# Optimization experiments

Measured on AMD Instinct MI355X. Metric: run time of the kernel, lower is better.

Reference implementation:

```python
import jax, jax.numpy as jnp
import numpy as np

D = 1024   # dim_embedding
H = 16     # n_head
HD = D // H


def setup_inputs() -> dict:
    key = jax.random.key(0)
    ks = jax.random.split(key, 5)
    B, T = 2, 2048
    x = jax.random.normal(ks[0], (B, T, D), dtype=jnp.float32)
    e = jax.random.normal(ks[1], (B, T, D), dtype=jnp.float32)
    s = 0.02
    W_en = jax.random.normal(ks[2], (D, 2 * D), dtype=jnp.float32) * s   # c_attn_en (k,v from encoder)
    W_q = jax.random.normal(ks[3], (D, D), dtype=jnp.float32) * s        # c_attn (q from decoder)
    W_o = jax.random.normal(ks[4], (D, D), dtype=jnp.float32) * s        # c_proj
    return {"x": x, "e": e, "W_en": W_en, "W_q": W_q, "W_o": W_o}


def reference(x, e, W_en, W_q, W_o):
    B, T, C = e.shape
    kv = e @ W_en                       # [B,T,2C]
    k, v = jnp.split(kv, 2, axis=-1)    # [B,T,C] each
    q = x @ W_q                         # [B,T,C]
    # reshape to heads: [B,H,T,hd]
    q = q.reshape(B, T, H, HD).transpose(0, 2, 1, 3)
    k = k.reshape(B, T, H, HD).transpose(0, 2, 1, 3)
    v = v.reshape(B, T, H, HD).transpose(0, 2, 1, 3)
    att = jnp.einsum("bhqd,bhkd->bhqk", q, k) * (1.0 / jnp.sqrt(jnp.float32(HD)))
    att = jax.nn.softmax(att, axis=-1)  # dropout=0 (eval)
    y = jnp.einsum("bhqk,bhkd->bhqd", att, v)
    y = y.transpose(0, 2, 1, 3).reshape(B, T, C)
    return y @ W_o
```

## Files before the change

### kernel.cpp

```cpp
#include <hip/hip_runtime.h>

typedef unsigned short u16;
typedef unsigned int u32;
typedef __bf16 bf16x8 __attribute__((ext_vector_type(8)));
typedef float f32x4 __attribute__((ext_vector_type(4)));
typedef float f32x16 __attribute__((ext_vector_type(16)));

#define D_EMB 1024
#define T_SEQ 2048
#define NH 16
#define HD 64

#define GLB(p) ((const __attribute__((address_space(1))) unsigned int*)(p))
#define LDSP(p) ((__attribute__((address_space(3))) unsigned int*)(p))

__device__ __forceinline__ u16 f2bf(float f) {
  union { float f; unsigned u; } c; c.f = f;
  unsigned u = c.u;
  unsigned r = (u + 0x7FFFu + ((u >> 16) & 1u)) >> 16;
  return (u16)r;
}
__device__ __forceinline__ u32 fbits(float f) {
  union { float f; unsigned u; } c; c.f = f; return c.u;
}

__global__ __launch_bounds__(256) void prep_kernel(
    const float* __restrict__ x, const float* __restrict__ e,
    const float* __restrict__ W_q, const float* __restrict__ W_en, const float* __restrict__ W_o,
    u16* __restrict__ xb, u16* __restrict__ eb,
    u16* __restrict__ Wqt, u16* __restrict__ Went, u16* __restrict__ Wot) {
  __shared__ float tile[32][33];
  const int bid = blockIdx.x, tid = threadIdx.x;
  if (bid < 8192) {
    const float* in = (bid < 4096) ? x : e;
    u16* out = (bid < 4096) ? xb : eb;
    int i = (bid & 4095) * 256 + tid;
    float4 v = reinterpret_cast<const float4*>(in)[i];
    ushort4 o;
    o.x = f2bf(v.x); o.y = f2bf(v.y); o.z = f2bf(v.z); o.w = f2bf(v.w);
    reinterpret_cast<ushort4*>(out)[i] = o;
    return;
  }
  const float* in; u16* out; int K, N, bx, by;
  int rem = bid - 8192;
  if (rem < 1024)      { in = W_q;  out = Wqt;  K = 1024; N = 1024; bx = rem & 31; by = rem >> 5; }
  else if (rem < 3072) { int r2 = rem - 1024; in = W_en; out = Went; K = 1024; N = 2048; bx = r2 & 63; by = r2 >> 6; }
  else                 { int r3 = rem - 3072; in = W_o;  out = Wot;  K = 1024; N = 1024; bx = r3 & 31; by = r3 >> 5; }
  int tx = tid & 31, ty = tid >> 5;
  int n0 = bx * 32, k0 = by * 32;
#pragma unroll
  for (int s = 0; s < 4; s++)
    tile[ty + 8 * s][tx] = in[(size_t)(k0 + ty + 8 * s) * N + n0 + tx];
  __syncthreads();
#pragma unroll
  for (int s = 0; s < 4; s++)
    out[(size_t)(n0 + ty + 8 * s) * K + k0 + tx] = f2bf(tile[tx][ty + 8 * s]);
}

__global__ __launch_bounds__(256) void proj_kernel(
    const u16* __restrict__ xb, const u16* __restrict__ eb,
    const u16* __restrict__ Wqt, const u16* __restrict__ Went,
    u16* __restrict__ qw, u16* __restrict__ kw, u16* __restrict__ vTw) {
  __shared__ u16 Al0[128 * 32], Bl0[128 * 32];
  __shared__ u16 Al1[128 * 32], Bl1[128 * 32];
  const int tid = threadIdx.x;
  const int nb = blockIdx.x, mb = blockIdx.y;
  const int wave = tid >> 6, lane = tid & 63;
  const int ln15 = lane & 15, quad = lane >> 4;
  const int wm = wave & 1, wn = wave >> 1;

  const u16* A = (nb < 8) ? xb : eb;
  const u16* Wt = (nb < 8) ? (Wqt + (size_t)nb * 128 * D_EMB)
                           : (Went + ((size_t)nb * 128 - D_EMB) * D_EMB);

  const int srow = lane >> 2, sch = lane & 3;
  const int gch = sch ^ ((srow >> 1) & 3);
  const u16* gA = A + (size_t)(mb * 128 + wave * 32 + srow) * D_EMB + gch * 8;
  const u16* gB = Wt + (size_t)(wave * 32 + srow) * D_EMB + gch * 8;

  auto stage = [&](int kb, u16* AL, u16* BL) {
    char* lA = (char*)AL + wave * 2048;
    char* lB = (char*)BL + wave * 2048;
#pragma unroll
    for (int it = 0; it < 2; it++) {
      __builtin_amdgcn_global_load_lds(GLB(gA + (size_t)it * 16 * D_EMB + kb), LDSP(lA + it * 1024), 16, 0, 0);
      __builtin_amdgcn_global_load_lds(GLB(gB + (size_t)it * 16 * D_EMB + kb), LDSP(lB + it * 1024), 16, 0, 0);
    }
  };

  f32x4 acc[4][4] = {};

  auto compute = [&](const u16* AL, const u16* BL) {
    bf16x8 af[4], bfr[4];
#pragma unroll
    for (int mt = 0; mt < 4; mt++) {
      int r = wm * 64 + mt * 16 + ln15;
      af[mt] = *reinterpret_cast<const bf16x8*>(&AL[r * 32 + ((quad ^ ((r >> 1) & 3)) * 8)]);
    }
#pragma unroll
    for (int nt = 0; nt < 4; nt++) {
      int r = wn * 64 + nt * 16 + ln15;
      bfr[nt] = *reinterpret_cast<const bf16x8*>(&BL[r * 32 + ((quad ^ ((r >> 1) & 3)) * 8)]);
    }
#pragma unroll
    for (int mt = 0; mt < 4; mt++)
#pragma unroll
      for (int nt = 0; nt < 4; nt++)
        acc[mt][nt] = __builtin_amdgcn_mfma_f32_16x16x32_bf16(af[mt], bfr[nt], acc[mt][nt], 0, 0, 0);
  };

  stage(0, Al0, Bl0);
  for (int kb = 0; kb < D_EMB; kb += 64) {
    __syncthreads();
    stage(kb + 32, Al1, Bl1);
    compute(Al0, Bl0);
    __syncthreads();
    if (kb + 64 < D_EMB) stage(kb + 64, Al0, Bl0);
    compute(Al1, Bl1);
  }

  const float QSCL = 0.125f * 1.44269504f;
#pragma unroll
  for (int mt = 0; mt < 4; mt++) {
#pragma unroll
    for (int nt = 0; nt < 4; nt++) {
#pragma unroll
      for (int i = 0; i < 4; i++) {
        int rr = mb * 128 + wm * 64 + mt * 16 + quad * 4 + i;
        int c  = nb * 128 + wn * 64 + nt * 16 + ln15;
        float v = acc[mt][nt][i];
        int b = rr >> 11, t = rr & 2047;
        if (c < D_EMB) {
          int h = c >> 6, d = c & 63;
          qw[(((size_t)(b * NH + h)) * T_SEQ + t) * HD + d] = f2bf(v * QSCL);
        } else if (c < 2 * D_EMB) {
          int cc = c - D_EMB; int h = cc >> 6, d = cc & 63;
          kw[(((size_t)(b * NH + h)) * T_SEQ + t) * HD + d] = f2bf(v);
        } else {
          int cc = c - 2 * D_EMB; int h = cc >> 6, d = cc & 63;
          vTw[(((size_t)(b * NH + h)) * HD + d) * T_SEQ + t] = f2bf(v);
        }
      }
    }
  }
}

__global__ __launch_bounds__(256) void attn_kernel(
    const u16* __restrict__ q, const u16* __restrict__ k,
    const u16* __restrict__ vT, u16* __restrict__ y) {
  __shared__ u16 Kl0[64][64], Vl0[64][64];
  __shared__ u16 Kl1[64][64], Vl1[64][64];
  __shared__ u16 Pl[4][32][64];

  const int bh = blockIdx.y;
  const int qt = blockIdx.x;
  const int tid = threadIdx.x;
  const int wave = tid >> 6, lane = tid & 63;
  const int q32 = lane & 31, hi = lane >> 5;
  const int b = bh >> 4, h = bh & 15;

  const int qrow = qt * 128 + wave * 32 + q32;
  const u16* qbase = q + ((size_t)bh * T_SEQ + qrow) * HD;
  bf16x8 qf[4];
#pragma unroll
  for (int s = 0; s < 4; s++)
    qf[s] = *reinterpret_cast<const bf16x8*>(qbase + s * 16 + hi * 8);

  f32x16 o2[2] = {};
  float lp = 0.f;

  const int srow = (lane >> 3) & 7;
  const int gch  = (lane & 7) ^ srow;
  const u16* kg0 = k  + ((size_t)bh * T_SEQ + wave * 16 + srow) * HD + gch * 8;
  const u16* vg0 = vT + ((size_t)bh * HD + wave * 16 + srow) * T_SEQ + gch * 8;

  auto issue_dma = [&](int t, u16 (*KL)[64], u16 (*VL)[64]) {
    char* klb = (char*)KL + wave * 2048;
    char* vlb = (char*)VL + wave * 2048;
    const u16* kp = kg0 + (size_t)t * 64 * HD;
    const u16* vp = vg0 + t * 64;
    __builtin_amdgcn_global_load_lds(GLB(kp),             LDSP(klb),        16, 0, 0);
    __builtin_amdgcn_global_load_lds(GLB(kp + 8 * HD),    LDSP(klb + 1024), 16, 0, 0);
    __builtin_amdgcn_global_load_lds(GLB(vp),             LDSP(vlb),        16, 0, 0);
    __builtin_amdgcn_global_load_lds(GLB(vp + 8 * T_SEQ), LDSP(vlb + 1024), 16, 0, 0);
  };

  auto body = [&](const u16 (*KL)[64], const u16 (*VL)[64]) {
    f32x16 s2[2] = {};
#pragma unroll
    for (int s = 0; s < 4; s++)
#pragma unroll
      for (int kt2 = 0; kt2 < 2; kt2++) {
        int r = kt2 * 32 + q32;
        bf16x8 kf = *reinterpret_cast<const bf16x8*>(&KL[r][(((s * 2 + hi) ^ (r & 7)) * 8)]);
        s2[kt2] = __builtin_amdgcn_mfma_f32_32x32x16_bf16(kf, qf[s], s2[kt2], 0, 0, 0);
      }

#pragma unroll
    for (int kt2 = 0; kt2 < 2; kt2++)
#pragma unroll
      for (int g = 0; g < 4; g++) {
        float p0 = __builtin_amdgcn_exp2f(s2[kt2][4 * g + 0]);
        float p1 = __builtin_amdgcn_exp2f(s2[kt2][4 * g + 1]);
        float p2 = __builtin_amdgcn_exp2f(s2[kt2][4 * g + 2]);
        float p3 = __builtin_amdgcn_exp2f(s2[kt2][4 * g + 3]);
        lp += (p0 + p1) + (p2 + p3);
        u32 dw0 = __builtin_amdgcn_perm(fbits(p1), fbits(p0), 0x07060302u);
        u32 dw1 = __builtin_amdgcn_perm(fbits(p3), fbits(p2), 0x07060302u);
        int phys = (kt2 * 4 + g) ^ (q32 & 7);
        *reinterpret_cast<uint2*>(&Pl[wave][q32][phys * 8 + 4 * hi]) = make_uint2(dw0, dw1);
      }
    asm volatile("s_waitcnt lgkmcnt(0)" ::: "memory");

#pragma unroll
    for (int s = 0; s < 4; s++) {
      bf16x8 pf = *reinterpret_cast<const bf16x8*>(
          &Pl[wave][q32][(((s * 2 + hi) ^ (q32 & 7)) * 8)]);
#pragma unroll
      for (int dt = 0; dt < 2; dt++) {
        int r = dt * 32 + q32;
        bf16x8 vf = *reinterpret_cast<const bf16x8*>(&VL[r][(((s * 2 + hi) ^ (r & 7)) * 8)]);
        o2[dt] = __builtin_amdgcn_mfma_f32_32x32x16_bf16(vf, pf, o2[dt], 0, 0, 0);
      }
    }
  };

  issue_dma(0, Kl0, Vl0);
  for (int t = 0; t < 32; t += 2) {
    __syncthreads();
    issue_dma(t + 1, Kl1, Vl1);
    body(Kl0, Vl0);
    __syncthreads();
    if (t + 2 < 32) issue_dma(t + 2, Kl0, Vl0);
    body(Kl1, Vl1);
  }

  lp += __shfl_xor(lp, 32, 64);
  const float inv = 1.0f / lp;

  const size_t ybase = ((size_t)b * T_SEQ + qrow) * D_EMB + h * 64;
#pragma unroll
  for (int dt = 0; dt < 2; dt++)
#pragma unroll
    for (int g = 0; g < 4; g++) {
      u16 b0 = f2bf(o2[dt][4 * g + 0] * inv), b1 = f2bf(o2[dt][4 * g + 1] * inv);
      u16 b2 = f2bf(o2[dt][4 * g + 2] * inv), b3 = f2bf(o2[dt][4 * g + 3] * inv);
      u32 dw0 = (u32)b0 | ((u32)b1 << 16);
      u32 dw1 = (u32)b2 | ((u32)b3 << 16);
      *reinterpret_cast<uint2*>(&y[ybase + dt * 32 + 8 * g + 4 * hi]) = make_uint2(dw0, dw1);
    }
}

__global__ __launch_bounds__(256) void oproj_kernel(
    const u16* __restrict__ yw, const u16* __restrict__ Wot, float* __restrict__ out) {
  __shared__ u16 Al0[64 * 32], Al1[64 * 32];
  __shared__ u16 Bl0[128 * 32], Bl1[128 * 32];
  const int tid = threadIdx.x;
  const int nb = blockIdx.x, mb = blockIdx.y;
  const int wave = tid >> 6, lane = tid & 63;
  const int ln15 = lane & 15, quad = lane >> 4;
  const int wm = wave & 1, wn = wave >> 1;

  const int srow = lane >> 2, sch = lane & 3;
  const int gch = sch ^ ((srow >> 1) & 3);
  const u16* gA = yw  + (size_t)(mb * 64 + wave * 16 + srow) * D_EMB + gch * 8;
  const u16* gB = Wot + (size_t)(nb * 128 + wave * 32 + srow) * D_EMB + gch * 8;

  auto stage = [&](int kb, u16* AL, u16* BL) {
    char* lA = (char*)AL + wave * 1024;
    char* lB = (char*)BL + wave * 2048;
    __builtin_amdgcn_global_load_lds(GLB(gA + kb), LDSP(lA), 16, 0, 0);
#pragma unroll
    for (int it = 0; it < 2; it++)
      __builtin_amdgcn_global_load_lds(GLB(gB + (size_t)it * 16 * D_EMB + kb), LDSP(lB + it * 1024), 16, 0, 0);
  };

  f32x4 acc[2][4] = {};

  auto compute = [&](const u16* AL, const u16* BL) {
    bf16x8 af[2], bfr[4];
#pragma unroll
    for (int mt = 0; mt < 2; mt++) {
      int r = wm * 32 + mt * 16 + ln15;
      af[mt] = *reinterpret_cast<const bf16x8*>(&AL[r * 32 + ((quad ^ ((r >> 1) & 3)) * 8)]);
    }
#pragma unroll
    for (int nt = 0; nt < 4; nt++) {
      int r = wn * 64 + nt * 16 + ln15;
      bfr[nt] = *reinterpret_cast<const bf16x8*>(&BL[r * 32 + ((quad ^ ((r >> 1) & 3)) * 8)]);
    }
#pragma unroll
    for (int mt = 0; mt < 2; mt++)
#pragma unroll
      for (int nt = 0; nt < 4; nt++)
        acc[mt][nt] = __builtin_amdgcn_mfma_f32_16x16x32_bf16(af[mt], bfr[nt], acc[mt][nt], 0, 0, 0);
  };

  stage(0, Al0, Bl0);
  for (int kb = 0; kb < D_EMB; kb += 64) {
    __syncthreads();
    stage(kb + 32, Al1, Bl1);
    compute(Al0, Bl0);
    __syncthreads();
    if (kb + 64 < D_EMB) stage(kb + 64, Al0, Bl0);
    compute(Al1, Bl1);
  }

#pragma unroll
  for (int mt = 0; mt < 2; mt++)
#pragma unroll
    for (int nt = 0; nt < 4; nt++)
#pragma unroll
      for (int i = 0; i < 4; i++) {
        int rr = mb * 64 + wm * 32 + mt * 16 + quad * 4 + i;
        int c  = nb * 128 + wn * 64 + nt * 16 + ln15;
        out[(size_t)rr * D_EMB + c] = acc[mt][nt][i];
      }
}

extern "C" void kernel_launch(void* const* d_in, const int* in_sizes, int n_in,
                              void* d_out, int out_size, void* d_ws, size_t ws_size,
                              hipStream_t stream) {
  const float* x    = (const float*)d_in[0];
  const float* e    = (const float*)d_in[1];
  const float* W_en = (const float*)d_in[2];
  const float* W_q  = (const float*)d_in[3];
  const float* W_o  = (const float*)d_in[4];
  float* out = (float*)d_out;

  char* w = (char*)d_ws;
  u16* xb   = (u16*)(w);
  u16* eb   = (u16*)(w + (8u  << 20));
  u16* Wqt  = (u16*)(w + (16u << 20));
  u16* Went = (u16*)(w + (18u << 20));
  u16* Wot  = (u16*)(w + (22u << 20));
  u16* qw   = (u16*)(w + (24u << 20));
  u16* kw   = (u16*)(w + (32u << 20));
  u16* vT   = (u16*)(w + (40u << 20));
  u16* yw   = (u16*)(w + (48u << 20));

  prep_kernel<<<12288, 256, 0, stream>>>(x, e, W_q, W_en, W_o, xb, eb, Wqt, Went, Wot);
  proj_kernel<<<dim3(24, 32), 256, 0, stream>>>(xb, eb, Wqt, Went, qw, kw, vT);
  attn_kernel<<<dim3(T_SEQ / 128, 32), 256, 0, stream>>>(qw, kw, vT, yw);
  oproj_kernel<<<dim3(8, 64), 256, 0, stream>>>(yw, Wot, out);
}
```

Before: 203.3 us.

## Fuse prep, projection, attention and output projection into one persistent kernel

Replaces the four separate launches with a single persistent kernel of 768 blocks that runs each phase in turn, separated by software grid barriers built on atomic counters. The goal is to remove launch gaps and tail effects between the stages. This relies on all 768 blocks being co-resident (launch bounds of 3 blocks per CU with 48KB of shared memory each), and if that fails the kernel deadlocks. In the attention and output-projection phases only 512 of the 768 blocks do work, and the y buffer now reuses the xb workspace region.

```diff
diff --git a/kernel.cpp b/kernel.cpp
--- a/kernel.cpp
+++ b/kernel.cpp
@@ -10,6 +10,7 @@
 #define T_SEQ 2048
 #define NH 16
 #define HD 64
+#define GRID_N 768u
 
 #define GLB(p) ((const __attribute__((address_space(1))) unsigned int*)(p))
 #define LDSP(p) ((__attribute__((address_space(3))) unsigned int*)(p))
@@ -24,298 +25,309 @@
   union { float f; unsigned u; } c; c.f = f; return c.u;
 }
 
-__global__ __launch_bounds__(256) void prep_kernel(
+__device__ __forceinline__ void gridbar(u32* cnt, u32 target) {
+  __syncthreads();
+  if (threadIdx.x == 0) {
+    __hip_atomic_fetch_add(cnt, 1u, __ATOMIC_RELEASE, __HIP_MEMORY_SCOPE_AGENT);
+    while (__hip_atomic_load(cnt, __ATOMIC_ACQUIRE, __HIP_MEMORY_SCOPE_AGENT) < target)
+      __builtin_amdgcn_s_sleep(8);
+  }
+  __syncthreads();
+}
+
+__global__ __launch_bounds__(256, 3) void mega_kernel(
     const float* __restrict__ x, const float* __restrict__ e,
     const float* __restrict__ W_q, const float* __restrict__ W_en, const float* __restrict__ W_o,
     u16* __restrict__ xb, u16* __restrict__ eb,
-    u16* __restrict__ Wqt, u16* __restrict__ Went, u16* __restrict__ Wot) {
-  __shared__ float tile[32][33];
-  const int bid = blockIdx.x, tid = threadIdx.x;
-  if (bid < 8192) {
-    const float* in = (bid < 4096) ? x : e;
-    u16* out = (bid < 4096) ? xb : eb;
-    int i = (bid & 4095) * 256 + tid;
-    float4 v = reinterpret_cast<const float4*>(in)[i];
-    ushort4 o;
-    o.x = f2bf(v.x); o.y = f2bf(v.y); o.z = f2bf(v.z); o.w = f2bf(v.w);
-    reinterpret_cast<ushort4*>(out)[i] = o;
-    return;
-  }
-  const float* in; u16* out; int K, N, bx, by;
-  int rem = bid - 8192;
-  if (rem < 1024)      { in = W_q;  out = Wqt;  K = 1024; N = 1024; bx = rem & 31; by = rem >> 5; }
-  else if (rem < 3072) { int r2 = rem - 1024; in = W_en; out = Went; K = 1024; N = 2048; bx = r2 & 63; by = r2 >> 6; }
-  else                 { int r3 = rem - 3072; in = W_o;  out = Wot;  K = 1024; N = 1024; bx = r3 & 31; by = r3 >> 5; }
-  int tx = tid & 31, ty = tid >> 5;
-  int n0 = bx * 32, k0 = by * 32;
-#pragma unroll
-  for (int s = 0; s < 4; s++)
-    tile[ty + 8 * s][tx] = in[(size_t)(k0 + ty + 8 * s) * N + n0 + tx];
-  __syncthreads();
-#pragma unroll
-  for (int s = 0; s < 4; s++)
-    out[(size_t)(n0 + ty + 8 * s) * K + k0 + tx] = f2bf(tile[tx][ty + 8 * s]);
-}
-
-__global__ __launch_bounds__(256) void proj_kernel(
-    const u16* __restrict__ xb, const u16* __restrict__ eb,
-    const u16* __restrict__ Wqt, const u16* __restrict__ Went,
-    u16* __restrict__ qw, u16* __restrict__ kw, u16* __restrict__ vTw) {
-  __shared__ u16 Al0[128 * 32], Bl0[128 * 32];
-  __shared__ u16 Al1[128 * 32], Bl1[128 * 32];
+    u16* __restrict__ Wqt, u16* __restrict__ Went, u16* __restrict__ Wot,
+    u16* __restrict__ qw, u16* __restrict__ kw, u16* __restrict__ vTw,
+    u16* __restrict__ yw, float* __restrict__ out, u32* __restrict__ bar) {
+  __shared__ __align__(16) char smem[49152];
+  const int bid = blockIdx.x;
   const int tid = threadIdx.x;
-  const int nb = blockIdx.x, mb = blockIdx.y;
   const int wave = tid >> 6, lane = tid & 63;
   const int ln15 = lane & 15, quad = lane >> 4;
-  const int wm = wave & 1, wn = wave >> 1;
-
-  const u16* A = (nb < 8) ? xb : eb;
-  const u16* Wt = (nb < 8) ? (Wqt + (size_t)nb * 128 * D_EMB)
-                           : (Went + ((size_t)nb * 128 - D_EMB) * D_EMB);
-
-  const int srow = lane >> 2, sch = lane & 3;
-  const int gch = sch ^ ((srow >> 1) & 3);
-  const u16* gA = A + (size_t)(mb * 128 + wave * 32 + srow) * D_EMB + gch * 8;
-  const u16* gB = Wt + (size_t)(wave * 32 + srow) * D_EMB + gch * 8;
-
-  auto stage = [&](int kb, u16* AL, u16* BL) {
-    char* lA = (char*)AL + wave * 2048;
-    char* lB = (char*)BL + wave * 2048;
-#pragma unroll
-    for (int it = 0; it < 2; it++) {
-      __builtin_amdgcn_global_load_lds(GLB(gA + (size_t)it * 16 * D_EMB + kb), LDSP(lA + it * 1024), 16, 0, 0);
-      __builtin_amdgcn_global_load_lds(GLB(gB + (size_t)it * 16 * D_EMB + kb), LDSP(lB + it * 1024), 16, 0, 0);
-    }
-  };
-
-  f32x4 acc[4][4] = {};
-
-  auto compute = [&](const u16* AL, const u16* BL) {
-    bf16x8 af[4], bfr[4];
+
+  {
+    float* tile = (float*)smem;
+    for (u32 u = (u32)bid; u < 12288u; u += GRID_N) {
+      if (u < 8192u) {
+        const float* in = (u < 4096u) ? x : e;
+        u16* outp = (u < 4096u) ? xb : eb;
+        int i = (int)(u & 4095u) * 256 + tid;
+        float4 v = reinterpret_cast<const float4*>(in)[i];
+        ushort4 o;
+        o.x = f2bf(v.x); o.y = f2bf(v.y); o.z = f2bf(v.z); o.w = f2bf(v.w);
+        reinterpret_cast<ushort4*>(outp)[i] = o;
+      } else {
+        const float* in; u16* outp; int K, N, bx, by;
+        int rem = (int)u - 8192;
+        if (rem < 1024)      { in = W_q;  outp = Wqt;  K = 1024; N = 1024; bx = rem & 31; by = rem >> 5; }
+        else if (rem < 3072) { int r2 = rem - 1024; in = W_en; outp = Went; K = 1024; N = 2048; bx = r2 & 63; by = r2 >> 6; }
+        else                 { int r3 = rem - 3072; in = W_o;  outp = Wot;  K = 1024; N = 1024; bx = r3 & 31; by = r3 >> 5; }
+        int tx = tid & 31, ty = tid >> 5;
+        int n0 = bx * 32, k0 = by * 32;
+        __syncthreads();
+#pragma unroll
+        for (int s = 0; s < 4; s++)
+          tile[(ty + 8 * s) * 33 + tx] = in[(size_t)(k0 + ty + 8 * s) * N + n0 + tx];
+        __syncthreads();
+#pragma unroll
+        for (int s = 0; s < 4; s++)
+          outp[(size_t)(n0 + ty + 8 * s) * K + k0 + tx] = f2bf(tile[tx * 33 + ty + 8 * s]);
+      }
+    }
+  }
+  gridbar(bar, GRID_N);
+
+  {
+    u16* Al0 = (u16*)(smem);
+    u16* Bl0 = (u16*)(smem + 8192);
+    u16* Al1 = (u16*)(smem + 16384);
+    u16* Bl1 = (u16*)(smem + 24576);
+    const int nb = bid % 24, mb = bid / 24;
+    const int wm = wave & 1, wn = wave >> 1;
+
+    const u16* A = (nb < 8) ? xb : eb;
+    const u16* Wt = (nb < 8) ? (Wqt + (size_t)nb * 128 * D_EMB)
+                             : (Went + ((size_t)nb * 128 - D_EMB) * D_EMB);
+
+    const int srow = lane >> 2, sch = lane & 3;
+    const int gch = sch ^ ((srow >> 1) & 3);
+    const u16* gA = A + (size_t)(mb * 128 + wave * 32 + srow) * D_EMB + gch * 8;
+    const u16* gB = Wt + (size_t)(wave * 32 + srow) * D_EMB + gch * 8;
+
+    auto stage = [&](int kb, u16* AL, u16* BL) {
+      char* lA = (char*)AL + wave * 2048;
+      char* lB = (char*)BL + wave * 2048;
+#pragma unroll
+      for (int it = 0; it < 2; it++) {
+        __builtin_amdgcn_global_load_lds(GLB(gA + (size_t)it * 16 * D_EMB + kb), LDSP(lA + it * 1024), 16, 0, 0);
+        __builtin_amdgcn_global_load_lds(GLB(gB + (size_t)it * 16 * D_EMB + kb), LDSP(lB + it * 1024), 16, 0, 0);
+      }
+    };
+
+    f32x4 acc[4][4] = {};
+    auto compute = [&](const u16* AL, const u16* BL) {
+      bf16x8 af[4], bfr[4];
+#pragma unroll
+      for (int mt = 0; mt < 4; mt++) {
+        int r = wm * 64 + mt * 16 + ln15;
+        af[mt] = *reinterpret_cast<const bf16x8*>(&AL[r * 32 + ((quad ^ ((r >> 1) & 3)) * 8)]);
+      }
+#pragma unroll
+      for (int nt = 0; nt < 4; nt++) {
+        int r = wn * 64 + nt * 16 + ln15;
+        bfr[nt] = *reinterpret_cast<const bf16x8*>(&BL[r * 32 + ((quad ^ ((r >> 1) & 3)) * 8)]);
+      }
+#pragma unroll
+      for (int mt = 0; mt < 4; mt++)
+#pragma unroll
+        for (int nt = 0; nt < 4; nt++)
+          acc[mt][nt] = __builtin_amdgcn_mfma_f32_16x16x32_bf16(af[mt], bfr[nt], acc[mt][nt], 0, 0, 0);
+    };
+
+    stage(0, Al0, Bl0);
+    for (int kb = 0; kb < D_EMB; kb += 64) {
+      __syncthreads();
+      stage(kb + 32, Al1, Bl1);
+      compute(Al0, Bl0);
+      __syncthreads();
+      if (kb + 64 < D_EMB) stage(kb + 64, Al0, Bl0);
+      compute(Al1, Bl1);
+    }
+
+    const float QSCL = 0.125f * 1.44269504f;
 #pragma unroll
     for (int mt = 0; mt < 4; mt++) {
-      int r = wm * 64 + mt * 16 + ln15;
-      af[mt] = *reinterpret_cast<const bf16x8*>(&AL[r * 32 + ((quad ^ ((r >> 1) & 3)) * 8)]);
-    }
-#pragma unroll
-    for (int nt = 0; nt < 4; nt++) {
-      int r = wn * 64 + nt * 16 + ln15;
-      bfr[nt] = *reinterpret_cast<const bf16x8*>(&BL[r * 32 + ((quad ^ ((r >> 1) & 3)) * 8)]);
-    }
-#pragma unroll
-    for (int mt = 0; mt < 4; mt++)
+#pragma unroll
+      for (int nt = 0; nt < 4; nt++) {
+#pragma unroll
+        for (int i = 0; i < 4; i++) {
+          int rr = mb * 128 + wm * 64 + mt * 16 + quad * 4 + i;
+          int c  = nb * 128 + wn * 64 + nt * 16 + ln15;
+          float v = acc[mt][nt][i];
+          int b = rr >> 11, t = rr & 2047;
+          if (c < D_EMB) {
+            int h = c >> 6, d = c & 63;
+            qw[(((size_t)(b * NH + h)) * T_SEQ + t) * HD + d] = f2bf(v * QSCL);
+          } else if (c < 2 * D_EMB) {
+            int cc = c - D_EMB; int h = cc >> 6, d = cc & 63;
+            kw[(((size_t)(b * NH + h)) * T_SEQ + t) * HD + d] = f2bf(v);
+          } else {
+            int cc = c - 2 * D_EMB; int h = cc >> 6, d = cc & 63;
+            vTw[(((size_t)(b * NH + h)) * HD + d) * T_SEQ + t] = f2bf(v);
+          }
+        }
+      }
+    }
+  }
+  gridbar(bar, 2 * GRID_N);
+
+  if (bid < 512) {
+    u16 (*Kl0)[64] = (u16(*)[64])(smem);
+    u16 (*Vl0)[64] = (u16(*)[64])(smem + 8192);
+    u16 (*Kl1)[64] = (u16(*)[64])(smem + 16384);
+    u16 (*Vl1)[64] = (u16(*)[64])(smem + 24576);
+    u16* Pl = (u16*)(smem + 32768);
+
+    const int qt = bid & 15, bh = bid >> 4;
+    const int q32 = lane & 31, hi = lane >> 5;
+    const int b = bh >> 4, h = bh & 15;
+
+    const int qrow = qt * 128 + wave * 32 + q32;
+    const u16* qbase = qw + ((size_t)bh * T_SEQ + qrow) * HD;
+    bf16x8 qf[4];
+#pragma unroll
+    for (int s = 0; s < 4; s++)
+      qf[s] = *reinterpret_cast<const bf16x8*>(qbase + s * 16 + hi * 8);
+
+    f32x16 o2[2] = {};
+    float lp = 0.f;
+
+    const int srow = (lane >> 3) & 7;
+    const int gch  = (lane & 7) ^ srow;
+    const u16* kg0 = kw  + ((size_t)bh * T_SEQ + wave * 16 + srow) * HD + gch * 8;
+    const u16* vg0 = vTw + ((size_t)bh * HD + wave * 16 + srow) * T_SEQ + gch * 8;
+
+    auto issue_dma = [&](int t, u16 (*KL)[64], u16 (*VL)[64]) {
+      char* klb = (char*)KL + wave * 2048;
+      char* vlb = (char*)VL + wave * 2048;
+      const u16* kp = kg0 + (size_t)t * 64 * HD;
+      const u16* vp = vg0 + t * 64;
+      __builtin_amdgcn_global_load_lds(GLB(kp),             LDSP(klb),        16, 0, 0);
+      __builtin_amdgcn_global_load_lds(GLB(kp + 8 * HD),    LDSP(klb + 1024), 16, 0, 0);
+      __builtin_amdgcn_global_load_lds(GLB(vp),             LDSP(vlb),        16, 0, 0);
+      __builtin_amdgcn_global_load_lds(GLB(vp + 8 * T_SEQ), LDSP(vlb + 1024), 16, 0, 0);
+    };
+
+    auto body = [&](const u16 (*KL)[64], const u16 (*VL)[64]) {
+      f32x16 s2[2] = {};
+#pragma unroll
+      for (int s = 0; s < 4; s++)
+#pragma unroll
+        for (int kt2 = 0; kt2 < 2; kt2++) {
+          int r = kt2 * 32 + q32;
+          bf16x8 kf = *reinterpret_cast<const bf16x8*>(&KL[r][(((s * 2 + hi) ^ (r & 7)) * 8)]);
+          s2[kt2] = __builtin_amdgcn_mfma_f32_32x32x16_bf16(kf, qf[s], s2[kt2], 0, 0, 0);
+        }
+#pragma unroll
+      for (int kt2 = 0; kt2 < 2; kt2++)
+#pragma unroll
+        for (int g = 0; g < 4; g++) {
+          float p0 = __builtin_amdgcn_exp2f(s2[kt2][4 * g + 0]);
+          float p1 = __builtin_amdgcn_exp2f(s2[kt2][4 * g + 1]);
+          float p2 = __builtin_amdgcn_exp2f(s2[kt2][4 * g + 2]);
+          float p3 = __builtin_amdgcn_exp2f(s2[kt2][4 * g + 3]);
+          lp += (p0 + p1) + (p2 + p3);
+          u32 dw0 = __builtin_amdgcn_perm(fbits(p1), fbits(p0), 0x07060302u);
+          u32 dw1 = __builtin_amdgcn_perm(fbits(p3), fbits(p2), 0x07060302u);
+          int phys = (kt2 * 4 + g) ^ (q32 & 7);
+          *reinterpret_cast<uint2*>(&Pl[(wave * 32 + q32) * 64 + phys * 8 + 4 * hi]) = make_uint2(dw0, dw1);
+        }
+      asm volatile("s_waitcnt lgkmcnt(0)" ::: "memory");
+#pragma unroll
+      for (int s = 0; s < 4; s++) {
+        bf16x8 pf = *reinterpret_cast<const bf16x8*>(
+            &Pl[(wave * 32 + q32) * 64 + (((s * 2 + hi) ^ (q32 & 7)) * 8)]);
+#pragma unroll
+        for (int dt = 0; dt < 2; dt++) {
+          int r = dt * 32 + q32;
+          bf16x8 vf = *reinterpret_cast<const bf16x8*>(&VL[r][(((s * 2 + hi) ^ (r & 7)) * 8)]);
+          o2[dt] = __builtin_amdgcn_mfma_f32_32x32x16_bf16(vf, pf, o2[dt], 0, 0, 0);
+        }
+      }
+    };
+
+    issue_dma(0, Kl0, Vl0);
+    for (int t = 0; t < 32; t += 2) {
+      __syncthreads();
+      issue_dma(t + 1, Kl1, Vl1);
+      body(Kl0, Vl0);
+      __syncthreads();
+      if (t + 2 < 32) issue_dma(t + 2, Kl0, Vl0);
+      body(Kl1, Vl1);
+    }
+
+    lp += __shfl_xor(lp, 32, 64);
+    const float inv = 1.0f / lp;
+    const size_t ybase = ((size_t)b * T_SEQ + qrow) * D_EMB + h * 64;
+#pragma unroll
+    for (int dt = 0; dt < 2; dt++)
+#pragma unroll
+      for (int g = 0; g < 4; g++) {
+        u16 b0 = f2bf(o2[dt][4 * g + 0] * inv), b1 = f2bf(o2[dt][4 * g + 1] * inv);
+        u16 b2 = f2bf(o2[dt][4 * g + 2] * inv), b3 = f2bf(o2[dt][4 * g + 3] * inv);
+        u32 dw0 = (u32)b0 | ((u32)b1 << 16);
+        u32 dw1 = (u32)b2 | ((u32)b3 << 16);
+        *reinterpret_cast<uint2*>(&yw[ybase + dt * 32 + 8 * g + 4 * hi]) = make_uint2(dw0, dw1);
+      }
+  }
+  gridbar(bar, 3 * GRID_N);
+
+  if (bid < 512) {
+    u16* Al0 = (u16*)(smem);
+    u16* Al1 = (u16*)(smem + 4096);
+    u16* Bl0 = (u16*)(smem + 8192);
+    u16* Bl1 = (u16*)(smem + 16384);
+    const int nb = bid & 7, mb = bid >> 3;
+    const int wm = wave & 1, wn = wave >> 1;
+
+    const int srow = lane >> 2, sch = lane & 3;
+    const int gch = sch ^ ((srow >> 1) & 3);
+    const u16* gA = yw  + (size_t)(mb * 64 + wave * 16 + srow) * D_EMB + gch * 8;
+    const u16* gB = Wot + (size_t)(nb * 128 + wave * 32 + srow) * D_EMB + gch * 8;
+
+    auto stage = [&](int kb, u16* AL, u16* BL) {
+      char* lA = (char*)AL + wave * 1024;
+      char* lB = (char*)BL + wave * 2048;
+      __builtin_amdgcn_global_load_lds(GLB(gA + kb), LDSP(lA), 16, 0, 0);
+#pragma unroll
+      for (int it = 0; it < 2; it++)
+        __builtin_amdgcn_global_load_lds(GLB(gB + (size_t)it * 16 * D_EMB + kb), LDSP(lB + it * 1024), 16, 0, 0);
+    };
+
+    f32x4 acc[2][4] = {};
+    auto compute = [&](const u16* AL, const u16* BL) {
+      bf16x8 af[2], bfr[4];
+#pragma unroll
+      for (int mt = 0; mt < 2; mt++) {
+        int r = wm * 32 + mt * 16 + ln15;
+        af[mt] = *reinterpret_cast<const bf16x8*>(&AL[r * 32 + ((quad ^ ((r >> 1) & 3)) * 8)]);
+      }
+#pragma unroll
+      for (int nt = 0; nt < 4; nt++) {
+        int r = wn * 64 + nt * 16 + ln15;
+        bfr[nt] = *reinterpret_cast<const bf16x8*>(&BL[r * 32 + ((quad ^ ((r >> 1) & 3)) * 8)]);
+      }
+#pragma unroll
+      for (int mt = 0; mt < 2; mt++)
+#pragma unroll
+        for (int nt = 0; nt < 4; nt++)
+          acc[mt][nt] = __builtin_amdgcn_mfma_f32_16x16x32_bf16(af[mt], bfr[nt], acc[mt][nt], 0, 0, 0);
+    };
+
+    stage(0, Al0, Bl0);
+    for (int kb = 0; kb < D_EMB; kb += 64) {
+      __syncthreads();
+      stage(kb + 32, Al1, Bl1);
+      compute(Al0, Bl0);
+      __syncthreads();
+      if (kb + 64 < D_EMB) stage(kb + 64, Al0, Bl0);
+      compute(Al1, Bl1);
+    }
+
+#pragma unroll
+    for (int mt = 0; mt < 2; mt++)
 #pragma unroll
       for (int nt = 0; nt < 4; nt++)
-        acc[mt][nt] = __builtin_amdgcn_mfma_f32_16x16x32_bf16(af[mt], bfr[nt], acc[mt][nt], 0, 0, 0);
-  };
-
-  stage(0, Al0, Bl0);
-  for (int kb = 0; kb < D_EMB; kb += 64) {
-    __syncthreads();
-    stage(kb + 32, Al1, Bl1);
-    compute(Al0, Bl0);
-    __syncthreads();
-    if (kb + 64 < D_EMB) stage(kb + 64, Al0, Bl0);
-    compute(Al1, Bl1);
-  }
-
-  const float QSCL = 0.125f * 1.44269504f;
-#pragma unroll
-  for (int mt = 0; mt < 4; mt++) {
-#pragma unroll
-    for (int nt = 0; nt < 4; nt++) {
-#pragma unroll
-      for (int i = 0; i < 4; i++) {
-        int rr = mb * 128 + wm * 64 + mt * 16 + quad * 4 + i;
-        int c  = nb * 128 + wn * 64 + nt * 16 + ln15;
-        float v = acc[mt][nt][i];
-        int b = rr >> 11, t = rr & 2047;
-        if (c < D_EMB) {
-          int h = c >> 6, d = c & 63;
-          qw[(((size_t)(b * NH + h)) * T_SEQ + t) * HD + d] = f2bf(v * QSCL);
-        } else if (c < 2 * D_EMB) {
-          int cc = c - D_EMB; int h = cc >> 6, d = cc & 63;
-          kw[(((size_t)(b * NH + h)) * T_SEQ + t) * HD + d] = f2bf(v);
-        } else {
-          int cc = c - 2 * D_EMB; int h = cc >> 6, d = cc & 63;
-          vTw[(((size_t)(b * NH + h)) * HD + d) * T_SEQ + t] = f2bf(v);
-        }
-      }
-    }
-  }
-}
-
-__global__ __launch_bounds__(256) void attn_kernel(
-    const u16* __restrict__ q, const u16* __restrict__ k,
-    const u16* __restrict__ vT, u16* __restrict__ y) {
-  __shared__ u16 Kl0[64][64], Vl0[64][64];
-  __shared__ u16 Kl1[64][64], Vl1[64][64];
-  __shared__ u16 Pl[4][32][64];
-
-  const int bh = blockIdx.y;
-  const int qt = blockIdx.x;
-  const int tid = threadIdx.x;
-  const int wave = tid >> 6, lane = tid & 63;
-  const int q32 = lane & 31, hi = lane >> 5;
-  const int b = bh >> 4, h = bh & 15;
-
-  const int qrow = qt * 128 + wave * 32 + q32;
-  const u16* qbase = q + ((size_t)bh * T_SEQ + qrow) * HD;
-  bf16x8 qf[4];
-#pragma unroll
-  for (int s = 0; s < 4; s++)
-    qf[s] = *reinterpret_cast<const bf16x8*>(qbase + s * 16 + hi * 8);
-
-  f32x16 o2[2] = {};
-  float lp = 0.f;
-
-  const int srow = (lane >> 3) & 7;
-  const int gch  = (lane & 7) ^ srow;
-  const u16* kg0 = k  + ((size_t)bh * T_SEQ + wave * 16 + srow) * HD + gch * 8;
-  const u16* vg0 = vT + ((size_t)bh * HD + wave * 16 + srow) * T_SEQ + gch * 8;
-
-  auto issue_dma = [&](int t, u16 (*KL)[64], u16 (*VL)[64]) {
-    char* klb = (char*)KL + wave * 2048;
-    char* vlb = (char*)VL + wave * 2048;
-    const u16* kp = kg0 + (size_t)t * 64 * HD;
-    const u16* vp = vg0 + t * 64;
-    __builtin_amdgcn_global_load_lds(GLB(kp),             LDSP(klb),        16, 0, 0);
-    __builtin_amdgcn_global_load_lds(GLB(kp + 8 * HD),    LDSP(klb + 1024), 16, 0, 0);
-    __builtin_amdgcn_global_load_lds(GLB(vp),             LDSP(vlb),        16, 0, 0);
-    __builtin_amdgcn_global_load_lds(GLB(vp + 8 * T_SEQ), LDSP(vlb + 1024), 16, 0, 0);
-  };
-
-  auto body = [&](const u16 (*KL)[64], const u16 (*VL)[64]) {
-    f32x16 s2[2] = {};
-#pragma unroll
-    for (int s = 0; s < 4; s++)
-#pragma unroll
-      for (int kt2 = 0; kt2 < 2; kt2++) {
-        int r = kt2 * 32 + q32;
-        bf16x8 kf = *reinterpret_cast<const bf16x8*>(&KL[r][(((s * 2 + hi) ^ (r & 7)) * 8)]);
-        s2[kt2] = __builtin_amdgcn_mfma_f32_32x32x16_bf16(kf, qf[s], s2[kt2], 0, 0, 0);
-      }
-
-#pragma unroll
-    for (int kt2 = 0; kt2 < 2; kt2++)
-#pragma unroll
-      for (int g = 0; g < 4; g++) {
-        float p0 = __builtin_amdgcn_exp2f(s2[kt2][4 * g + 0]);
-        float p1 = __builtin_amdgcn_exp2f(s2[kt2][4 * g + 1]);
-        float p2 = __builtin_amdgcn_exp2f(s2[kt2][4 * g + 2]);
-        float p3 = __builtin_amdgcn_exp2f(s2[kt2][4 * g + 3]);
-        lp += (p0 + p1) + (p2 + p3);
-        u32 dw0 = __builtin_amdgcn_perm(fbits(p1), fbits(p0), 0x07060302u);
-        u32 dw1 = __builtin_amdgcn_perm(fbits(p3), fbits(p2), 0x07060302u);
-        int phys = (kt2 * 4 + g) ^ (q32 & 7);
-        *reinterpret_cast<uint2*>(&Pl[wave][q32][phys * 8 + 4 * hi]) = make_uint2(dw0, dw1);
-      }
-    asm volatile("s_waitcnt lgkmcnt(0)" ::: "memory");
-
-#pragma unroll
-    for (int s = 0; s < 4; s++) {
-      bf16x8 pf = *reinterpret_cast<const bf16x8*>(
-          &Pl[wave][q32][(((s * 2 + hi) ^ (q32 & 7)) * 8)]);
-#pragma unroll
-      for (int dt = 0; dt < 2; dt++) {
-        int r = dt * 32 + q32;
-        bf16x8 vf = *reinterpret_cast<const bf16x8*>(&VL[r][(((s * 2 + hi) ^ (r & 7)) * 8)]);
-        o2[dt] = __builtin_amdgcn_mfma_f32_32x32x16_bf16(vf, pf, o2[dt], 0, 0, 0);
-      }
-    }
-  };
-
-  issue_dma(0, Kl0, Vl0);
-  for (int t = 0; t < 32; t += 2) {
-    __syncthreads();
-    issue_dma(t + 1, Kl1, Vl1);
-    body(Kl0, Vl0);
-    __syncthreads();
-    if (t + 2 < 32) issue_dma(t + 2, Kl0, Vl0);
-    body(Kl1, Vl1);
-  }
-
-  lp += __shfl_xor(lp, 32, 64);
-  const float inv = 1.0f / lp;
-
-  const size_t ybase = ((size_t)b * T_SEQ + qrow) * D_EMB + h * 64;
-#pragma unroll
-  for (int dt = 0; dt < 2; dt++)
-#pragma unroll
-    for (int g = 0; g < 4; g++) {
-      u16 b0 = f2bf(o2[dt][4 * g + 0] * inv), b1 = f2bf(o2[dt][4 * g + 1] * inv);
-      u16 b2 = f2bf(o2[dt][4 * g + 2] * inv), b3 = f2bf(o2[dt][4 * g + 3] * inv);
-      u32 dw0 = (u32)b0 | ((u32)b1 << 16);
-      u32 dw1 = (u32)b2 | ((u32)b3 << 16);
-      *reinterpret_cast<uint2*>(&y[ybase + dt * 32 + 8 * g + 4 * hi]) = make_uint2(dw0, dw1);
-    }
-}
-
-__global__ __launch_bounds__(256) void oproj_kernel(
-    const u16* __restrict__ yw, const u16* __restrict__ Wot, float* __restrict__ out) {
-  __shared__ u16 Al0[64 * 32], Al1[64 * 32];
-  __shared__ u16 Bl0[128 * 32], Bl1[128 * 32];
-  const int tid = threadIdx.x;
-  const int nb = blockIdx.x, mb = blockIdx.y;
-  const int wave = tid >> 6, lane = tid & 63;
-  const int ln15 = lane & 15, quad = lane >> 4;
-  const int wm = wave & 1, wn = wave >> 1;
-
-  const int srow = lane >> 2, sch = lane & 3;
-  const int gch = sch ^ ((srow >> 1) & 3);
-  const u16* gA = yw  + (size_t)(mb * 64 + wave * 16 + srow) * D_EMB + gch * 8;
-  const u16* gB = Wot + (size_t)(nb * 128 + wave * 32 + srow) * D_EMB + gch * 8;
-
-  auto stage = [&](int kb, u16* AL, u16* BL) {
-    char* lA = (char*)AL + wave * 1024;
-    char* lB = (char*)BL + wave * 2048;
-    __builtin_amdgcn_global_load_lds(GLB(gA + kb), LDSP(lA), 16, 0, 0);
-#pragma unroll
-    for (int it = 0; it < 2; it++)
-      __builtin_amdgcn_global_load_lds(GLB(gB + (size_t)it * 16 * D_EMB + kb), LDSP(lB + it * 1024), 16, 0, 0);
-  };
-
-  f32x4 acc[2][4] = {};
-
-  auto compute = [&](const u16* AL, const u16* BL) {
-    bf16x8 af[2], bfr[4];
-#pragma unroll
-    for (int mt = 0; mt < 2; mt++) {
-      int r = wm * 32 + mt * 16 + ln15;
-      af[mt] = *reinterpret_cast<const bf16x8*>(&AL[r * 32 + ((quad ^ ((r >> 1) & 3)) * 8)]);
-    }
-#pragma unroll
-    for (int nt = 0; nt < 4; nt++) {
-      int r = wn * 64 + nt * 16 + ln15;
-      bfr[nt] = *reinterpret_cast<const bf16x8*>(&BL[r * 32 + ((quad ^ ((r >> 1) & 3)) * 8)]);
-    }
-#pragma unroll
-    for (int mt = 0; mt < 2; mt++)
-#pragma unroll
-      for (int nt = 0; nt < 4; nt++)
-        acc[mt][nt] = __builtin_amdgcn_mfma_f32_16x16x32_bf16(af[mt], bfr[nt], acc[mt][nt], 0, 0, 0);
-  };
-
-  stage(0, Al0, Bl0);
-  for (int kb = 0; kb < D_EMB; kb += 64) {
-    __syncthreads();
-    stage(kb + 32, Al1, Bl1);
-    compute(Al0, Bl0);
-    __syncthreads();
-    if (kb + 64 < D_EMB) stage(kb + 64, Al0, Bl0);
-    compute(Al1, Bl1);
-  }
-
-#pragma unroll
-  for (int mt = 0; mt < 2; mt++)
-#pragma unroll
-    for (int nt = 0; nt < 4; nt++)
-#pragma unroll
-      for (int i = 0; i < 4; i++) {
-        int rr = mb * 64 + wm * 32 + mt * 16 + quad * 4 + i;
-        int c  = nb * 128 + wn * 64 + nt * 16 + ln15;
-        out[(size_t)rr * D_EMB + c] = acc[mt][nt][i];
-      }
+#pragma unroll
+        for (int i = 0; i < 4; i++) {
+          int rr = mb * 64 + wm * 32 + mt * 16 + quad * 4 + i;
+          int c  = nb * 128 + wn * 64 + nt * 16 + ln15;
+          out[(size_t)rr * D_EMB + c] = acc[mt][nt][i];
+        }
+  }
 }
 
 extern "C" void kernel_launch(void* const* d_in, const int* in_sizes, int n_in,
@@ -330,6 +342,7 @@
 
   char* w = (char*)d_ws;
   u16* xb   = (u16*)(w);
+  u16* yw   = (u16*)(w);
   u16* eb   = (u16*)(w + (8u  << 20));
   u16* Wqt  = (u16*)(w + (16u << 20));
   u16* Went = (u16*)(w + (18u << 20));
@@ -337,10 +350,10 @@
   u16* qw   = (u16*)(w + (24u << 20));
   u16* kw   = (u16*)(w + (32u << 20));
   u16* vT   = (u16*)(w + (40u << 20));
-  u16* yw   = (u16*)(w + (48u << 20));
-
-  prep_kernel<<<12288, 256, 0, stream>>>(x, e, W_q, W_en, W_o, xb, eb, Wqt, Went, Wot);
-  proj_kernel<<<dim3(24, 32), 256, 0, stream>>>(xb, eb, Wqt, Went, qw, kw, vT);
-  attn_kernel<<<dim3(T_SEQ / 128, 32), 256, 0, stream>>>(qw, kw, vT, yw);
-  oproj_kernel<<<dim3(8, 64), 256, 0, stream>>>(yw, Wot, out);
-}
+  u32* bar  = (u32*)(w + (48u << 20));
+
+  hipMemsetAsync(bar, 0, 64, stream);
+  mega_kernel<<<GRID_N, 256, 0, stream>>>(x, e, W_q, W_en, W_o,
+                                          xb, eb, Wqt, Went, Wot,
+                                          qw, kw, vT, yw, out, bar);
+}
```

Result: slower. 585.0 us (+187.8%).
